# Kernel optimization log

Measured on AMD Instinct MI355X. Metric: run time of the kernel, lower is better.

Reference implementation:

```python
import jax, jax.numpy as jnp
import numpy as np

N_NODES = 100000
N_EDGES = 1250000
F_IN = 128
F_OUT = 64
N_GRAPHS = 256


def setup_inputs() -> dict:
    key = jax.random.key(0)
    k1, k2, k3, k4, k5 = jax.random.split(key, 5)
    node_feat = jax.random.normal(k1, (N_NODES, F_IN), dtype=jnp.float32)
    edge_index = jax.random.randint(k2, (2, N_EDGES), 0, N_NODES, dtype=jnp.int32)
    batch = jnp.sort(jax.random.randint(k3, (N_NODES,), 0, N_GRAPHS, dtype=jnp.int32))
    # PyG Linear weight layout: [out_channels, in_channels]; glorot-ish scale
    W = jax.random.normal(k4, (F_OUT, F_IN), dtype=jnp.float32) / np.sqrt(F_IN)
    b = jax.random.normal(k5, (F_OUT,), dtype=jnp.float32) * 0.01
    return {"node_feat": node_feat, "edge_index": edge_index, "batch": batch,
            "W": W, "b": b, "num_graphs": N_GRAPHS}


def reference(node_feat, edge_index, batch, W, b, num_graphs):
    n = node_feat.shape[0]
    # GCNConv: linear transform (no bias yet)
    x = node_feat @ W.T  # [N, F_OUT]
    # add self-loops (PyG default add_self_loops=True)
    loop = jnp.arange(n, dtype=edge_index.dtype)
    row = jnp.concatenate([edge_index[0], loop])  # source
    col = jnp.concatenate([edge_index[1], loop])  # target
    # symmetric normalization deg^{-1/2}[row] * deg^{-1/2}[col], deg over targets
    deg = jax.ops.segment_sum(jnp.ones_like(col, dtype=x.dtype), col, num_segments=n)
    dis = jnp.where(deg > 0, jax.lax.rsqrt(deg), 0.0)
    norm = dis[row] * dis[col]  # [E+N]
    # gather -> scale -> scatter-add, then bias
    agg = jax.ops.segment_sum(x[row] * norm[:, None], col, num_segments=n)
    out = jax.nn.relu(agg + b)
    # global_mean_pool over batch ids
    sums = jax.ops.segment_sum(out, batch, num_segments=num_graphs)
    counts = jax.ops.segment_sum(jnp.ones((n,), out.dtype), batch, num_segments=num_graphs)
    return sums / jnp.maximum(counts, 1.0)[:, None]
```

## Files before the change

### kernel.cpp

```cpp
#include <hip/hip_runtime.h>

#define N_NODES  100000
#define N_EDGES  1250000
#define F_IN     128
#define F_OUT    64
#define N_GRAPHS 256
#define NB_LIN   1563
#define NB_LINB  391
#define NBKT     782
#define NCHK     256
#define CHKSZ    4883
#define M_H      (NBKT * NCHK)
#define MB_H     196
#define BKT_CAP  2048

typedef __attribute__((ext_vector_type(8))) short short8;
typedef __attribute__((ext_vector_type(4))) float f32x4;

static __device__ __forceinline__ unsigned short f2bf(float f) {
    unsigned u = __builtin_bit_cast(unsigned, f);
    u += 0x7fff + ((u >> 16) & 1);
    return (unsigned short)(u >> 16);
}
static __device__ __forceinline__ float bf2f(unsigned short h) {
    unsigned u = ((unsigned)h) << 16;
    return __builtin_bit_cast(float, u);
}
static __device__ __forceinline__ float bflo(unsigned v) {
    return __builtin_bit_cast(float, v << 16);
}
static __device__ __forceinline__ float bfhi(unsigned v) {
    return __builtin_bit_cast(float, v & 0xffff0000u);
}

__global__ __launch_bounds__(256) void lin_hist_k(const float* __restrict__ x,
                                                  const float* __restrict__ W,
                                                  unsigned short* __restrict__ z,
                                                  const int* __restrict__ col,
                                                  int* __restrict__ H) {
    __shared__ unsigned xs[64 * 64];
    __shared__ unsigned ws[64 * 64];
    int tid = threadIdx.x;

    if (blockIdx.x >= NB_LINB) {
        int c = blockIdx.x - NB_LINB;
        int* cnt = (int*)xs;
        for (int b = tid; b < NBKT; b += 256) cnt[b] = 0;
        __syncthreads();
        int s = c * CHKSZ;
        int e = s + CHKSZ; if (e > N_EDGES) e = N_EDGES;
        for (int i = s + tid; i < e; i += 256)
            atomicAdd(&cnt[col[i] >> 7], 1);
        __syncthreads();
        for (int b = tid; b < NBKT; b += 256)
            H[b * NCHK + c] = cnt[b];
        return;
    }

    #pragma unroll
    for (int rr = 0; rr < 8; ++rr) {
        int idx = rr * 256 + tid;
        int n = idx >> 5, q = idx & 31;
        int d   = (n << 6) + (q << 1);
        int sdw = (n & 7) << 2;
        const float4 wv = *(const float4*)(W + (size_t)n * F_IN + q * 4);
        ws[(d ^ sdw)]     = (unsigned)f2bf(wv.x) | ((unsigned)f2bf(wv.y) << 16);
        ws[(d ^ sdw) + 1] = (unsigned)f2bf(wv.z) | ((unsigned)f2bf(wv.w) << 16);
    }

    int lane = tid & 63;
    int wv_  = tid >> 6;
    int m0   = wv_ << 4;
    int lr   = lane & 15;
    int lg   = lane >> 4;

    for (int t4 = 0; t4 < 4; ++t4) {
        int tile = blockIdx.x * 4 + t4;
        if (tile >= NB_LIN) break;
        int base = tile * 64;
        int nmax = N_NODES - base; if (nmax > 64) nmax = 64;

        #pragma unroll
        for (int rr = 0; rr < 8; ++rr) {
            int idx = rr * 256 + tid;
            int n = idx >> 5, q = idx & 31;
            int d   = (n << 6) + (q << 1);
            int sdw = (n & 7) << 2;
            float4 xv = make_float4(0.f, 0.f, 0.f, 0.f);
            if (n < nmax) xv = *(const float4*)(x + (size_t)(base + n) * F_IN + q * 4);
            xs[(d ^ sdw)]     = (unsigned)f2bf(xv.x) | ((unsigned)f2bf(xv.y) << 16);
            xs[(d ^ sdw) + 1] = (unsigned)f2bf(xv.z) | ((unsigned)f2bf(xv.w) << 16);
        }
        __syncthreads();

        f32x4 acc0 = (f32x4)(0.f), acc1 = (f32x4)(0.f);
        f32x4 acc2 = (f32x4)(0.f), acc3 = (f32x4)(0.f);

        #pragma unroll
        for (int t = 0; t < 4; ++t) {
            int nn = m0 + lr;
            int da = ((nn << 6) + (t << 4) + (lg << 2)) ^ ((nn & 7) << 2);
            short8 a = *(const short8*)(xs + da);
            #pragma unroll
            for (int ff = 0; ff < 4; ++ff) {
                int f  = (ff << 4) + lr;
                int db = ((f << 6) + (t << 4) + (lg << 2)) ^ ((f & 7) << 2);
                short8 b = *(const short8*)(ws + db);
                f32x4 c = (ff == 0) ? acc0 : (ff == 1) ? acc1 : (ff == 2) ? acc2 : acc3;
                c = __builtin_amdgcn_mfma_f32_16x16x32_bf16(a, b, c, 0, 0, 0);
                if (ff == 0) acc0 = c; else if (ff == 1) acc1 = c;
                else if (ff == 2) acc2 = c; else acc3 = c;
            }
        }

        #pragma unroll
        for (int r = 0; r < 4; ++r) {
            int node = m0 + (lg << 2) + r;
            if (node < nmax) {
                size_t o = (size_t)(base + node) * F_OUT + lr;
                z[o +  0] = f2bf(acc0[r]);
                z[o + 16] = f2bf(acc1[r]);
                z[o + 32] = f2bf(acc2[r]);
                z[o + 48] = f2bf(acc3[r]);
            }
        }
        __syncthreads();
    }
}

__global__ __launch_bounds__(1024) void scanH1_k(int* __restrict__ H, int* __restrict__ bsum) {
    __shared__ int lds[1024];
    int tid = threadIdx.x;
    int i = blockIdx.x * 1024 + tid;
    int v = (i < M_H) ? H[i] : 0;
    lds[tid] = v;
    __syncthreads();
    for (int off = 1; off < 1024; off <<= 1) {
        int t = (tid >= off) ? lds[tid - off] : 0;
        __syncthreads();
        lds[tid] += t;
        __syncthreads();
    }
    if (i < M_H) H[i] = lds[tid] - v;
    if (tid == 1023) bsum[blockIdx.x] = lds[tid];
}

__global__ __launch_bounds__(256) void scanH2_k(int* __restrict__ bsum) {
    __shared__ int lds[256];
    int tid = threadIdx.x;
    int v = (tid < MB_H) ? bsum[tid] : 0;
    lds[tid] = v;
    __syncthreads();
    for (int off = 1; off < 256; off <<= 1) {
        int t = (tid >= off) ? lds[tid - off] : 0;
        __syncthreads();
        lds[tid] += t;
        __syncthreads();
    }
    if (tid < MB_H) bsum[tid] = lds[tid] - v;
}

__global__ __launch_bounds__(1024) void scanH3_k(int* __restrict__ H, const int* __restrict__ bsum) {
    int i = blockIdx.x * 1024 + threadIdx.x;
    if (i < M_H) H[i] += bsum[blockIdx.x];
}

__global__ __launch_bounds__(256) void scatter_k(const int* __restrict__ row,
                                                 const int* __restrict__ col,
                                                 const int* __restrict__ Hs,
                                                 int2* __restrict__ part) {
    __shared__ int cur[NBKT];
    int c = blockIdx.x, tid = threadIdx.x;
    for (int b = tid; b < NBKT; b += 256) cur[b] = Hs[b * NCHK + c];
    __syncthreads();
    int s = c * CHKSZ;
    int e = s + CHKSZ; if (e > N_EDGES) e = N_EDGES;
    for (int i = s + tid; i < e; i += 256) {
        int cc = col[i], rr = row[i];
        int p = atomicAdd(&cur[cc >> 7], 1);
        part[p] = make_int2(rr, cc);
    }
}

__global__ __launch_bounds__(256) void csr_k(const int* __restrict__ Hs,
                                             const int2* __restrict__ part,
                                             int* __restrict__ bucketF,
                                             int* __restrict__ deg,
                                             int* __restrict__ offs,
                                             float* __restrict__ dis,
                                             unsigned* __restrict__ z32) {
    __shared__ int rowL[BKT_CAP];
    __shared__ int colL[BKT_CAP];
    __shared__ int cnt[128], offsL[128], curL[128], scanT[128];
    __shared__ float disL[128];
    int b = blockIdx.x, tid = threadIdx.x;
    int s = Hs[b * NCHK];
    int e = (b < NBKT - 1) ? Hs[(b + 1) * NCHK] : N_EDGES;
    int m = e - s;

    if (tid < 128) cnt[tid] = 0;
    __syncthreads();
    for (int i = tid; i < m; i += 256) {
        int2 pr = part[s + i];
        rowL[i] = pr.x;
        int cl = pr.y & 127;
        colL[i] = cl;
        atomicAdd(&cnt[cl], 1);
    }
    __syncthreads();
    if (tid < 128) scanT[tid] = cnt[tid];
    __syncthreads();
    for (int off = 1; off < 128; off <<= 1) {
        int v = (tid < 128 && tid >= off) ? scanT[tid - off] : 0;
        __syncthreads();
        if (tid < 128) scanT[tid] += v;
        __syncthreads();
    }
    if (tid < 128) {
        int ex = scanT[tid] - cnt[tid];
        offsL[tid] = ex;
        curL[tid]  = ex;
        float d = rsqrtf((float)cnt[tid] + 1.0f);
        disL[tid] = d;
        int node = b * 128 + tid;
        if (node < N_NODES) {
            deg[node]  = cnt[tid];
            offs[node] = s + ex;
            dis[node]  = d;
        }
    }
    __syncthreads();
    for (int i = tid; i < m; i += 256) {
        int cl = colL[i];
        int p = atomicAdd(&curL[cl], 1);
        bucketF[s + p] = rowL[i];
    }
    int node = tid >> 1, half = tid & 1;
    int gnode = b * 128 + node;
    if (gnode < N_NODES) {
        float d = disL[node];
        unsigned* zp = z32 + (size_t)gnode * 32 + half * 16;
        #pragma unroll
        for (int k = 0; k < 16; ++k) {
            unsigned v = zp[k];
            zp[k] = (unsigned)f2bf(d * bflo(v)) | ((unsigned)f2bf(d * bfhi(v)) << 16);
        }
    }
}

__global__ __launch_bounds__(256) void gather_pool_k(const unsigned short* __restrict__ y,
                                                     const int* __restrict__ offs,
                                                     const int* __restrict__ deg,
                                                     const int* __restrict__ bucket,
                                                     const float* __restrict__ dis,
                                                     const int* __restrict__ batch,
                                                     const float* __restrict__ bias,
                                                     float* __restrict__ psum,
                                                     int* __restrict__ pcnt) {
    int lane = threadIdx.x & 63;
    int wid  = threadIdx.x >> 6;
    int i0   = (blockIdx.x * 4 + wid) * 8;
    int eo   = lane >> 5;
    int fp   = lane & 31;
    float bx = bias[2 * fp], by = bias[2 * fp + 1];

    int   om = (lane < 8) ? offs[i0 + lane]  : 0;
    int   dm = (lane < 8) ? deg[i0 + lane]   : 0;
    float sm = (lane < 8) ? dis[i0 + lane]   : 0.f;
    int   gm = (lane < 8) ? batch[i0 + lane] : 0;

    float rx = 0.f, ry = 0.f;
    int cur = -1, runlen = 0;
    #pragma unroll
    for (int n = 0; n < 8; ++n) {
        int i = i0 + n;
        int s = __shfl(om, n);
        int e = s + __shfl(dm, n);

        unsigned sv = *(const unsigned*)(y + (size_t)i * F_OUT + 2 * fp);
        float ax = (eo == 0) ? bflo(sv) : 0.f;
        float ay = (eo == 0) ? bfhi(sv) : 0.f;

        for (int j = s; j < e; j += 16) {
            #pragma unroll
            for (int u = 0; u < 8; ++u) {
                int id  = j + 2 * u + eo;
                int idc = (id < e) ? id : e - 1;
                int r   = bucket[idc];
                unsigned w = *(const unsigned*)(y + (size_t)r * F_OUT + 2 * fp);
                float wx = bflo(w), wy = bfhi(w);
                ax += (id < e) ? wx : 0.f;
                ay += (id < e) ? wy : 0.f;
            }
        }
        ax += __shfl_xor(ax, 32);
        ay += __shfl_xor(ay, 32);

        float di = __shfl(sm, n);
        float vx = fmaxf(fmaf(di, ax, bx), 0.f);
        float vy = fmaxf(fmaf(di, ay, by), 0.f);
        int g = __shfl(gm, n);
        if (g != cur) {
            if (cur >= 0 && eo == 0) {
                atomicAdd(&psum[cur * F_OUT + 2 * fp],     rx);
                atomicAdd(&psum[cur * F_OUT + 2 * fp + 1], ry);
                if (lane == 0) atomicAdd(&pcnt[cur], runlen);
            }
            cur = g; rx = 0.f; ry = 0.f; runlen = 0;
        }
        rx += vx; ry += vy; runlen++;
    }
    if (cur >= 0 && eo == 0) {
        atomicAdd(&psum[cur * F_OUT + 2 * fp],     rx);
        atomicAdd(&psum[cur * F_OUT + 2 * fp + 1], ry);
        if (lane == 0) atomicAdd(&pcnt[cur], runlen);
    }
}

__global__ __launch_bounds__(256) void final_k(const float* __restrict__ psum,
                                               const int* __restrict__ pcnt,
                                               float* __restrict__ out) {
    int t = blockIdx.x * blockDim.x + threadIdx.x;
    if (t < N_GRAPHS * F_OUT) {
        int g = t >> 6;
        float c = (float)(pcnt[g] > 1 ? pcnt[g] : 1);
        out[t] = psum[t] / c;
    }
}

extern "C" void kernel_launch(void* const* d_in, const int* in_sizes, int n_in,
                              void* d_out, int out_size, void* d_ws, size_t ws_size,
                              hipStream_t stream) {
    const float* node_feat = (const float*)d_in[0];
    const int*   edges     = (const int*)d_in[1];
    const int*   batch     = (const int*)d_in[2];
    const float* W         = (const float*)d_in[3];
    const float* b         = (const float*)d_in[4];

    unsigned short* z = (unsigned short*)d_ws;
    int2*  part    = (int2*)(z + (size_t)N_NODES * F_OUT);
    int*   bucketF = (int*)(part + N_EDGES);
    int*   H       = bucketF + N_EDGES;
    int*   bsumH   = H + M_H;
    int*   deg     = bsumH + 256;
    int*   offs    = deg + N_NODES;
    float* dis     = (float*)(offs + N_NODES);
    float* psum    = dis + N_NODES;
    int*   pcnt    = (int*)(psum + N_GRAPHS * F_OUT);

    hipMemsetAsync(psum, 0, ((size_t)N_GRAPHS * F_OUT + N_GRAPHS) * 4, stream);

    const int* row = edges;
    const int* col = edges + N_EDGES;

    lin_hist_k<<<NB_LINB + NCHK, 256, 0, stream>>>(node_feat, W, z, col, H);
    scanH1_k<<<MB_H, 1024, 0, stream>>>(H, bsumH);
    scanH2_k<<<1, 256, 0, stream>>>(bsumH);
    scanH3_k<<<MB_H, 1024, 0, stream>>>(H, bsumH);
    scatter_k<<<NCHK, 256, 0, stream>>>(row, col, H, part);
    csr_k<<<NBKT, 256, 0, stream>>>(H, part, bucketF, deg, offs, dis, (unsigned*)z);
    gather_pool_k<<<N_NODES / 32, 256, 0, stream>>>(z, offs, deg, bucketF,
                                                    dis, batch, b, psum, pcnt);
    final_k<<<(N_GRAPHS * F_OUT + 255) / 256, 256, 0, stream>>>(psum, pcnt, (float*)d_out);
}
```

Before: 119.2 us.

## Co-schedule linear transform with edge scatter and batch gather loads

Moves the bf16 MFMA linear-transform blocks out of the histogram kernel and into the scatter kernel. The histogram then runs alone, and the GEMM overlaps with the memory-bound scatter instead. In gather_pool_k the neighbor loop now issues all eight bucket index loads, then all eight row loads, then accumulates, which exposes more memory-level parallelism. It also adds an occupancy hint to launch_bounds. The scatter blocks now allocate the larger 32KB shared footprint, which may reduce their occupancy.

```diff
diff --git a/kernel.cpp b/kernel.cpp
--- a/kernel.cpp
+++ b/kernel.cpp
@@ -33,29 +33,86 @@
     return __builtin_bit_cast(float, v & 0xffff0000u);
 }
 
-__global__ __launch_bounds__(256) void lin_hist_k(const float* __restrict__ x,
-                                                  const float* __restrict__ W,
-                                                  unsigned short* __restrict__ z,
-                                                  const int* __restrict__ col,
-                                                  int* __restrict__ H) {
-    __shared__ unsigned xs[64 * 64];
-    __shared__ unsigned ws[64 * 64];
+__global__ __launch_bounds__(256) void hist_k(const int* __restrict__ col,
+                                              int* __restrict__ H) {
+    __shared__ int cnt[NBKT];
+    int c = blockIdx.x, tid = threadIdx.x;
+    for (int b = tid; b < NBKT; b += 256) cnt[b] = 0;
+    __syncthreads();
+    int s = c * CHKSZ;
+    int e = s + CHKSZ; if (e > N_EDGES) e = N_EDGES;
+    for (int i = s + tid; i < e; i += 256)
+        atomicAdd(&cnt[col[i] >> 7], 1);
+    __syncthreads();
+    for (int b = tid; b < NBKT; b += 256)
+        H[b * NCHK + c] = cnt[b];
+}
+
+__global__ __launch_bounds__(1024) void scanH1_k(int* __restrict__ H, int* __restrict__ bsum) {
+    __shared__ int lds[1024];
     int tid = threadIdx.x;
-
-    if (blockIdx.x >= NB_LINB) {
-        int c = blockIdx.x - NB_LINB;
-        int* cnt = (int*)xs;
-        for (int b = tid; b < NBKT; b += 256) cnt[b] = 0;
+    int i = blockIdx.x * 1024 + tid;
+    int v = (i < M_H) ? H[i] : 0;
+    lds[tid] = v;
+    __syncthreads();
+    for (int off = 1; off < 1024; off <<= 1) {
+        int t = (tid >= off) ? lds[tid - off] : 0;
+        __syncthreads();
+        lds[tid] += t;
+        __syncthreads();
+    }
+    if (i < M_H) H[i] = lds[tid] - v;
+    if (tid == 1023) bsum[blockIdx.x] = lds[tid];
+}
+
+__global__ __launch_bounds__(256) void scanH2_k(int* __restrict__ bsum) {
+    __shared__ int lds[256];
+    int tid = threadIdx.x;
+    int v = (tid < MB_H) ? bsum[tid] : 0;
+    lds[tid] = v;
+    __syncthreads();
+    for (int off = 1; off < 256; off <<= 1) {
+        int t = (tid >= off) ? lds[tid - off] : 0;
+        __syncthreads();
+        lds[tid] += t;
+        __syncthreads();
+    }
+    if (tid < MB_H) bsum[tid] = lds[tid] - v;
+}
+
+__global__ __launch_bounds__(1024) void scanH3_k(int* __restrict__ H, const int* __restrict__ bsum) {
+    int i = blockIdx.x * 1024 + threadIdx.x;
+    if (i < M_H) H[i] += bsum[blockIdx.x];
+}
+
+__global__ __launch_bounds__(256) void scatter_lin_k(const int* __restrict__ row,
+                                                     const int* __restrict__ col,
+                                                     const int* __restrict__ Hs,
+                                                     int2* __restrict__ part,
+                                                     const float* __restrict__ x,
+                                                     const float* __restrict__ W,
+                                                     unsigned short* __restrict__ z) {
+    __shared__ unsigned smem[2 * 64 * 64];
+    int tid = threadIdx.x;
+
+    if (blockIdx.x < NCHK) {
+        int* cur = (int*)smem;
+        int c = blockIdx.x;
+        for (int b = tid; b < NBKT; b += 256) cur[b] = Hs[b * NCHK + c];
         __syncthreads();
         int s = c * CHKSZ;
         int e = s + CHKSZ; if (e > N_EDGES) e = N_EDGES;
-        for (int i = s + tid; i < e; i += 256)
-            atomicAdd(&cnt[col[i] >> 7], 1);
-        __syncthreads();
-        for (int b = tid; b < NBKT; b += 256)
-            H[b * NCHK + c] = cnt[b];
+        for (int i = s + tid; i < e; i += 256) {
+            int cc = col[i], rr = row[i];
+            int p = atomicAdd(&cur[cc >> 7], 1);
+            part[p] = make_int2(rr, cc);
+        }
         return;
     }
+
+    unsigned* xs = smem;
+    unsigned* ws = smem + 64 * 64;
+    int lb = blockIdx.x - NCHK;
 
     #pragma unroll
     for (int rr = 0; rr < 8; ++rr) {
@@ -75,7 +132,7 @@
     int lg   = lane >> 4;
 
     for (int t4 = 0; t4 < 4; ++t4) {
-        int tile = blockIdx.x * 4 + t4;
+        int tile = lb * 4 + t4;
         if (tile >= NB_LIN) break;
         int base = tile * 64;
         int nmax = N_NODES - base; if (nmax > 64) nmax = 64;
@@ -125,60 +182,6 @@
             }
         }
         __syncthreads();
-    }
-}
-
-__global__ __launch_bounds__(1024) void scanH1_k(int* __restrict__ H, int* __restrict__ bsum) {
-    __shared__ int lds[1024];
-    int tid = threadIdx.x;
-    int i = blockIdx.x * 1024 + tid;
-    int v = (i < M_H) ? H[i] : 0;
-    lds[tid] = v;
-    __syncthreads();
-    for (int off = 1; off < 1024; off <<= 1) {
-        int t = (tid >= off) ? lds[tid - off] : 0;
-        __syncthreads();
-        lds[tid] += t;
-        __syncthreads();
-    }
-    if (i < M_H) H[i] = lds[tid] - v;
-    if (tid == 1023) bsum[blockIdx.x] = lds[tid];
-}
-
-__global__ __launch_bounds__(256) void scanH2_k(int* __restrict__ bsum) {
-    __shared__ int lds[256];
-    int tid = threadIdx.x;
-    int v = (tid < MB_H) ? bsum[tid] : 0;
-    lds[tid] = v;
-    __syncthreads();
-    for (int off = 1; off < 256; off <<= 1) {
-        int t = (tid >= off) ? lds[tid - off] : 0;
-        __syncthreads();
-        lds[tid] += t;
-        __syncthreads();
-    }
-    if (tid < MB_H) bsum[tid] = lds[tid] - v;
-}
-
-__global__ __launch_bounds__(1024) void scanH3_k(int* __restrict__ H, const int* __restrict__ bsum) {
-    int i = blockIdx.x * 1024 + threadIdx.x;
-    if (i < M_H) H[i] += bsum[blockIdx.x];
-}
-
-__global__ __launch_bounds__(256) void scatter_k(const int* __restrict__ row,
-                                                 const int* __restrict__ col,
-                                                 const int* __restrict__ Hs,
-                                                 int2* __restrict__ part) {
-    __shared__ int cur[NBKT];
-    int c = blockIdx.x, tid = threadIdx.x;
-    for (int b = tid; b < NBKT; b += 256) cur[b] = Hs[b * NCHK + c];
-    __syncthreads();
-    int s = c * CHKSZ;
-    int e = s + CHKSZ; if (e > N_EDGES) e = N_EDGES;
-    for (int i = s + tid; i < e; i += 256) {
-        int cc = col[i], rr = row[i];
-        int p = atomicAdd(&cur[cc >> 7], 1);
-        part[p] = make_int2(rr, cc);
     }
 }
 
@@ -248,21 +251,22 @@
     }
 }
 
-__global__ __launch_bounds__(256) void gather_pool_k(const unsigned short* __restrict__ y,
-                                                     const int* __restrict__ offs,
-                                                     const int* __restrict__ deg,
-                                                     const int* __restrict__ bucket,
-                                                     const float* __restrict__ dis,
-                                                     const int* __restrict__ batch,
-                                                     const float* __restrict__ bias,
-                                                     float* __restrict__ psum,
-                                                     int* __restrict__ pcnt) {
+__global__ __launch_bounds__(256, 4) void gather_pool_k(const unsigned short* __restrict__ y,
+                                                        const int* __restrict__ offs,
+                                                        const int* __restrict__ deg,
+                                                        const int* __restrict__ bucket,
+                                                        const float* __restrict__ dis,
+                                                        const int* __restrict__ batch,
+                                                        const float* __restrict__ bias,
+                                                        float* __restrict__ psum,
+                                                        int* __restrict__ pcnt) {
     int lane = threadIdx.x & 63;
     int wid  = threadIdx.x >> 6;
     int i0   = (blockIdx.x * 4 + wid) * 8;
     int eo   = lane >> 5;
     int fp   = lane & 31;
     float bx = bias[2 * fp], by = bias[2 * fp + 1];
+    const unsigned short* yb = y + 2 * fp;
 
     int   om = (lane < 8) ? offs[i0 + lane]  : 0;
     int   dm = (lane < 8) ? deg[i0 + lane]   : 0;
@@ -277,20 +281,27 @@
         int s = __shfl(om, n);
         int e = s + __shfl(dm, n);
 
-        unsigned sv = *(const unsigned*)(y + (size_t)i * F_OUT + 2 * fp);
+        unsigned sv = *(const unsigned*)(yb + (size_t)i * F_OUT);
         float ax = (eo == 0) ? bflo(sv) : 0.f;
         float ay = (eo == 0) ? bfhi(sv) : 0.f;
 
         for (int j = s; j < e; j += 16) {
+            int rr[8];
             #pragma unroll
             for (int u = 0; u < 8; ++u) {
-                int id  = j + 2 * u + eo;
-                int idc = (id < e) ? id : e - 1;
-                int r   = bucket[idc];
-                unsigned w = *(const unsigned*)(y + (size_t)r * F_OUT + 2 * fp);
-                float wx = bflo(w), wy = bfhi(w);
-                ax += (id < e) ? wx : 0.f;
-                ay += (id < e) ? wy : 0.f;
+                int id = j + 2 * u + eo;
+                rr[u] = bucket[(id < e) ? id : e - 1];
+            }
+            unsigned wv[8];
+            #pragma unroll
+            for (int u = 0; u < 8; ++u) {
+                unsigned w = *(const unsigned*)(yb + (size_t)rr[u] * F_OUT);
+                wv[u] = (j + 2 * u + eo < e) ? w : 0u;
+            }
+            #pragma unroll
+            for (int u = 0; u < 8; ++u) {
+                ax += bflo(wv[u]);
+                ay += bfhi(wv[u]);
             }
         }
         ax += __shfl_xor(ax, 32);
@@ -353,11 +364,12 @@
     const int* row = edges;
     const int* col = edges + N_EDGES;
 
-    lin_hist_k<<<NB_LINB + NCHK, 256, 0, stream>>>(node_feat, W, z, col, H);
+    hist_k<<<NCHK, 256, 0, stream>>>(col, H);
     scanH1_k<<<MB_H, 1024, 0, stream>>>(H, bsumH);
     scanH2_k<<<1, 256, 0, stream>>>(bsumH);
     scanH3_k<<<MB_H, 1024, 0, stream>>>(H, bsumH);
-    scatter_k<<<NCHK, 256, 0, stream>>>(row, col, H, part);
+    scatter_lin_k<<<NCHK + NB_LINB, 256, 0, stream>>>(row, col, H, part,
+                                                      node_feat, W, z);
     csr_k<<<NBKT, 256, 0, stream>>>(H, part, bucketF, deg, offs, dis, (unsigned*)z);
     gather_pool_k<<<N_NODES / 32, 256, 0, stream>>>(z, offs, deg, bucketF,
                                                     dis, batch, b, psum, pcnt);
```

Measured after the change: 118.8 us. No clear change (-0.4%).
